# Kernel optimization log

Measured on AMD Instinct MI355X. Metric: run time of the kernel, lower is better.

The kernel has to match this reference:

```python
import jax, jax.numpy as jnp
import numpy as np

B, T, D = 4, 2048, 1024
H, K, V = 4, 256, 256        # head_k_dim = head_v_dim = hidden/num_heads
M, TOPK = 256, 4             # num_slots == head_k_dim
CHUNK = 64                   # scan checkpointing granularity
SCALE = K ** -0.5            # kernel default q scale


def setup_inputs() -> dict:
    key = jax.random.key(0)
    ks = jax.random.split(key, 10)
    s = lambda i, shape, sc: jax.random.normal(ks[i], shape, jnp.float32) * sc
    return {
        "hidden_states": s(0, (B, T, D), 1.0),
        "Wq": s(1, (D, H * K), D ** -0.5),
        "Wk": s(2, (D, H * K), D ** -0.5),
        "Wv": s(3, (D, H * V), D ** -0.5),
        "Wa": s(4, (D, H), D ** -0.5),
        "Wr": s(5, (D, H * M), D ** -0.5),
        "Wb": s(6, (D, H), D ** -0.5),
        "dt": jax.random.uniform(ks[7], (H,), jnp.float32, np.log(0.001), np.log(0.1)),
        "norm_w": jnp.ones((V,), jnp.float32),
        "Wo": s(8, (H * V, D), (H * V) ** -0.5),
    }


def _l2norm(x):
    return x * jax.lax.rsqrt(jnp.sum(x * x, axis=-1, keepdims=True) + 1e-6)


def _delta_scan(q, k, v, g, beta):
    """Gated delta-rule recurrence. Time-major inputs:
    q,k,g: [T,B,H,K]; v: [T,B,H,V]; beta: [T,B,H]. Returns o: [T,B,H,V]."""
    def step(S, inp):
        qt, kt, vt, gt, bt = inp
        S = S * jnp.exp(gt)[..., None]                              # diag decay on key dim
        err = vt - jnp.einsum('bhk,bhkv->bhv', kt, S)               # delta-rule error
        S = S + kt[..., None] * (bt[..., None] * err)[..., None, :]
        o = jnp.einsum('bhk,bhkv->bhv', qt, S)
        return S, o

    @jax.checkpoint
    def chunk_fn(S, inp):
        return jax.lax.scan(step, S, inp)

    nc = T // CHUNK
    inp = tuple(x.reshape((nc, CHUNK) + x.shape[1:]) for x in (q, k, v, g, beta))
    S0 = jnp.zeros((B, H, K, V), jnp.float32)
    _, o = jax.lax.scan(chunk_fn, S0, inp)                          # o: [nc,CHUNK,B,H,V]
    return o.reshape((T,) + o.shape[2:])


def reference(hidden_states, Wq, Wk, Wv, Wa, Wr, Wb, dt, norm_w, Wo):
    h = hidden_states
    q = jax.nn.silu(h @ Wq).reshape(B, T, H, K)
    k = jax.nn.silu(h @ Wk).reshape(B, T, H, K)
    v = jax.nn.silu(h @ Wv).reshape(B, T, H, V)
    a = -jax.nn.softplus(h @ Wa) * jnp.exp(dt)                      # [B,T,H] log-decay magnitude
    rt = (h @ Wr).reshape(B, T, H, M)
    beta = jax.nn.sigmoid(h @ Wb)                                   # [B,T,H]

    # noisy top-k slot routing (eval: no noise)
    m = jax.nn.sigmoid(rt)
    w, idx = jax.lax.top_k(m, TOPK)                                 # [B,T,H,TOPK]
    mask = jnp.sum(jax.nn.one_hot(idx, M, dtype=m.dtype) * w[..., None], axis=-2)
    r = mask / (jnp.sum(mask, axis=-1, keepdims=True) + 1e-6)
    g = a[..., None] * r                                            # [B,T,H,K] (M == K)

    k = k * (1.0 - jnp.exp(g))
    q = _l2norm(q) * SCALE
    k = _l2norm(k)

    tm = lambda x: jnp.moveaxis(x, 1, 0)
    o = _delta_scan(tm(q), tm(k), tm(v), tm(g), tm(beta))           # [T,B,H,V]
    o = jnp.moveaxis(o, 0, 1)                                       # [B,T,H,V]

    # RMSNorm on head_v_dim (fp32, eps 1e-5)
    o = o * jax.lax.rsqrt(jnp.mean(o * o, axis=-1, keepdims=True) + 1e-5) * norm_w
    return o.reshape(B, T, H * V) @ Wo
```

## Files before the change

### kernel.cpp

```cpp
#include <hip/hip_runtime.h>
#include <hip/hip_bf16.h>

#define TT 2048
#define BB 4
#define HH 4
#define DD 1024

using bf16x8 = __attribute__((ext_vector_type(8))) short;
using f32x4  = __attribute__((ext_vector_type(4))) float;

__device__ __forceinline__ float wave_sum(float x) {
#pragma unroll
  for (int off = 32; off >= 1; off >>= 1) x += __shfl_xor(x, off);
  return x;
}

__device__ __forceinline__ float siluf(float x) {
  return x / (1.f + expf(-x));
}

__device__ __forceinline__ unsigned short f2bf(float f) {
  unsigned u = __float_as_uint(f);
  u = (u + 0x7fffu + ((u >> 16) & 1u)) >> 16;
  return (unsigned short)u;
}
__device__ __forceinline__ float bf2f(unsigned short b) {
  return __uint_as_float(((unsigned)b) << 16);
}
__device__ __forceinline__ unsigned pack2(float a, float b) {
  return ((unsigned)f2bf(a)) | (((unsigned)f2bf(b)) << 16);
}

__device__ __forceinline__ void gload_lds16(const void* g, void* l) {
  __builtin_amdgcn_global_load_lds(
      (const __attribute__((address_space(1))) unsigned int*)g,
      (__attribute__((address_space(3))) unsigned int*)l, 16, 0, 0);
}

#define LBAR()                                              \
  do {                                                      \
    asm volatile("s_waitcnt lgkmcnt(0)" ::: "memory");      \
    __builtin_amdgcn_s_barrier();                           \
    __builtin_amdgcn_sched_barrier(0);                      \
  } while (0)

__global__ __launch_bounds__(256) void gemm_bt(const unsigned short* __restrict__ A,
                                               const unsigned short* __restrict__ Bt,
                                               float* __restrict__ C,
                                               int M, int N, int K) {
  __shared__ unsigned short As[128 * 64];
  __shared__ unsigned short Bs[128 * 64];
  const int tid = threadIdx.x;
  const int l = tid & 63;
  const int w = tid >> 6;
  const int wm = w >> 1, wn = w & 1;
  const int bid = blockIdx.x;
  const int nt = N >> 7;
  const int swz = (bid & 7) * ((int)gridDim.x >> 3) + (bid >> 3);
  const int m0 = (swz / nt) * 128, n0 = (swz % nt) * 128;

  f32x4 acc[4][4];
#pragma unroll
  for (int i = 0; i < 4; ++i)
#pragma unroll
    for (int j = 0; j < 4; ++j) acc[i][j] = (f32x4){0.f, 0.f, 0.f, 0.f};

  size_t asrc[4], bsrc[4];
  int ldst[4];
#pragma unroll
  for (int it = 0; it < 4; ++it) {
    int chunk = (it * 4 + w) * 64 + l;
    int row = chunk >> 3, s = chunk & 7;
    size_t soff = (size_t)row * K + ((s ^ (row & 7)) << 3);
    asrc[it] = (size_t)m0 * K + soff;
    bsrc[it] = (size_t)n0 * K + soff;
    ldst[it] = chunk * 8;
  }
  int ra_off[2][4], rb_off[2][4];
#pragma unroll
  for (int kh = 0; kh < 2; ++kh)
#pragma unroll
    for (int f = 0; f < 4; ++f) {
      int rowA = wm * 64 + f * 16 + (l & 15);
      ra_off[kh][f] = rowA * 128 + (((kh * 4 + (l >> 4)) ^ (rowA & 7)) << 4);
      int rowB = wn * 64 + f * 16 + (l & 15);
      rb_off[kh][f] = rowB * 128 + (((kh * 4 + (l >> 4)) ^ (rowB & 7)) << 4);
    }

  for (int k0 = 0; k0 < K; k0 += 64) {
    __syncthreads();
#pragma unroll
    for (int it = 0; it < 4; ++it) {
      gload_lds16(A + asrc[it] + k0, As + ldst[it] - l * 8);
      gload_lds16(Bt + bsrc[it] + k0, Bs + ldst[it] - l * 8);
    }
    __syncthreads();
#pragma unroll
    for (int kh = 0; kh < 2; ++kh) {
      bf16x8 af[4], bfv[4];
#pragma unroll
      for (int f = 0; f < 4; ++f) {
        af[f] = *(const bf16x8*)((const char*)As + ra_off[kh][f]);
        bfv[f] = *(const bf16x8*)((const char*)Bs + rb_off[kh][f]);
      }
#pragma unroll
      for (int i = 0; i < 4; ++i)
#pragma unroll
        for (int j = 0; j < 4; ++j)
          acc[i][j] = __builtin_amdgcn_mfma_f32_16x16x32_bf16(af[i], bfv[j],
                                                              acc[i][j], 0, 0, 0);
    }
  }
  const int cn = n0 + wn * 64 + (l & 15);
  const int rbase = m0 + wm * 64 + ((l >> 4) << 2);
#pragma unroll
  for (int i = 0; i < 4; ++i)
#pragma unroll
    for (int j = 0; j < 4; ++j)
#pragma unroll
      for (int r = 0; r < 4; ++r)
        C[(size_t)(rbase + i * 16 + r) * N + cn + j * 16] = acc[i][j][r];
}

__global__ __launch_bounds__(256) void gemm_bt3(const unsigned short* __restrict__ Ah,
                                                const unsigned short* __restrict__ Al,
                                                const unsigned short* __restrict__ Bh,
                                                const unsigned short* __restrict__ Bl,
                                                float* __restrict__ C,
                                                int M, int N, int K) {
  __shared__ unsigned short Ash[128 * 64];
  __shared__ unsigned short Asl[128 * 64];
  __shared__ unsigned short Bsh[128 * 64];
  __shared__ unsigned short Bsl[128 * 64];
  const int tid = threadIdx.x;
  const int l = tid & 63;
  const int w = tid >> 6;
  const int wm = w >> 1, wn = w & 1;
  const int bid = blockIdx.x;
  const int nt = N >> 7;
  const int swz = (bid & 7) * ((int)gridDim.x >> 3) + (bid >> 3);
  const int m0 = (swz / nt) * 128, n0 = (swz % nt) * 128;

  f32x4 acc[4][4];
#pragma unroll
  for (int i = 0; i < 4; ++i)
#pragma unroll
    for (int j = 0; j < 4; ++j) acc[i][j] = (f32x4){0.f, 0.f, 0.f, 0.f};

  size_t asrc[4], bsrc[4];
  int ldst[4];
#pragma unroll
  for (int it = 0; it < 4; ++it) {
    int chunk = (it * 4 + w) * 64 + l;
    int row = chunk >> 3, s = chunk & 7;
    size_t soff = (size_t)row * K + ((s ^ (row & 7)) << 3);
    asrc[it] = (size_t)m0 * K + soff;
    bsrc[it] = (size_t)n0 * K + soff;
    ldst[it] = chunk * 8;
  }
  int ra_off[2][4], rb_off[2][4];
#pragma unroll
  for (int kh = 0; kh < 2; ++kh)
#pragma unroll
    for (int f = 0; f < 4; ++f) {
      int rowA = wm * 64 + f * 16 + (l & 15);
      ra_off[kh][f] = rowA * 128 + (((kh * 4 + (l >> 4)) ^ (rowA & 7)) << 4);
      int rowB = wn * 64 + f * 16 + (l & 15);
      rb_off[kh][f] = rowB * 128 + (((kh * 4 + (l >> 4)) ^ (rowB & 7)) << 4);
    }

  for (int k0 = 0; k0 < K; k0 += 64) {
    __syncthreads();
#pragma unroll
    for (int it = 0; it < 4; ++it) {
      gload_lds16(Ah + asrc[it] + k0, Ash + ldst[it] - l * 8);
      gload_lds16(Al + asrc[it] + k0, Asl + ldst[it] - l * 8);
      gload_lds16(Bh + bsrc[it] + k0, Bsh + ldst[it] - l * 8);
      gload_lds16(Bl + bsrc[it] + k0, Bsl + ldst[it] - l * 8);
    }
    __syncthreads();
#pragma unroll
    for (int kh = 0; kh < 2; ++kh) {
      bf16x8 afh[4], bfh[4], tmp[4];
#pragma unroll
      for (int f = 0; f < 4; ++f) {
        afh[f] = *(const bf16x8*)((const char*)Ash + ra_off[kh][f]);
        bfh[f] = *(const bf16x8*)((const char*)Bsh + rb_off[kh][f]);
      }
#pragma unroll
      for (int i = 0; i < 4; ++i)
#pragma unroll
        for (int j = 0; j < 4; ++j)
          acc[i][j] = __builtin_amdgcn_mfma_f32_16x16x32_bf16(afh[i], bfh[j],
                                                              acc[i][j], 0, 0, 0);
#pragma unroll
      for (int f = 0; f < 4; ++f)
        tmp[f] = *(const bf16x8*)((const char*)Asl + ra_off[kh][f]);
#pragma unroll
      for (int i = 0; i < 4; ++i)
#pragma unroll
        for (int j = 0; j < 4; ++j)
          acc[i][j] = __builtin_amdgcn_mfma_f32_16x16x32_bf16(tmp[i], bfh[j],
                                                              acc[i][j], 0, 0, 0);
#pragma unroll
      for (int f = 0; f < 4; ++f)
        tmp[f] = *(const bf16x8*)((const char*)Bsl + rb_off[kh][f]);
#pragma unroll
      for (int i = 0; i < 4; ++i)
#pragma unroll
        for (int j = 0; j < 4; ++j)
          acc[i][j] = __builtin_amdgcn_mfma_f32_16x16x32_bf16(afh[i], tmp[j],
                                                              acc[i][j], 0, 0, 0);
    }
  }
  const int cn = n0 + wn * 64 + (l & 15);
  const int rbase = m0 + wm * 64 + ((l >> 4) << 2);
#pragma unroll
  for (int i = 0; i < 4; ++i)
#pragma unroll
    for (int j = 0; j < 4; ++j)
#pragma unroll
      for (int r = 0; r < 4; ++r)
        C[(size_t)(rbase + i * 16 + r) * N + cn + j * 16] = acc[i][j][r];
}

__global__ __launch_bounds__(256) void cast2_bf16_kernel(const float* __restrict__ in,
                                                         unsigned short* __restrict__ hi,
                                                         unsigned short* __restrict__ lo) {
  const size_t i = ((size_t)blockIdx.x * 256 + threadIdx.x) * 4;
  float4 x = *(const float4*)(in + i);
  ushort4 h4, l4;
  h4.x = f2bf(x.x); l4.x = f2bf(x.x - bf2f(h4.x));
  h4.y = f2bf(x.y); l4.y = f2bf(x.y - bf2f(h4.y));
  h4.z = f2bf(x.z); l4.z = f2bf(x.z - bf2f(h4.z));
  h4.w = f2bf(x.w); l4.w = f2bf(x.w - bf2f(h4.w));
  *(ushort4*)(hi + i) = h4;
  *(ushort4*)(lo + i) = l4;
}

__global__ __launch_bounds__(256) void tcast_kernel(const float* __restrict__ W,
                                                    unsigned short* __restrict__ WT,
                                                    int R, int C) {
  __shared__ float tile[32][33];
  const int tx = threadIdx.x, ty = threadIdx.y;
  const int c0 = blockIdx.x * 32, r0 = blockIdx.y * 32;
#pragma unroll
  for (int i = 0; i < 4; ++i)
    tile[ty + 8 * i][tx] = W[(size_t)(r0 + ty + 8 * i) * C + c0 + tx];
  __syncthreads();
#pragma unroll
  for (int i = 0; i < 4; ++i)
    WT[(size_t)(c0 + ty + 8 * i) * R + r0 + tx] = f2bf(tile[tx][ty + 8 * i]);
}

__global__ __launch_bounds__(256) void tcast2_kernel(const float* __restrict__ W,
                                                     unsigned short* __restrict__ WTh,
                                                     unsigned short* __restrict__ WTl,
                                                     int R, int C) {
  __shared__ float tile[32][33];
  const int tx = threadIdx.x, ty = threadIdx.y;
  const int c0 = blockIdx.x * 32, r0 = blockIdx.y * 32;
#pragma unroll
  for (int i = 0; i < 4; ++i)
    tile[ty + 8 * i][tx] = W[(size_t)(r0 + ty + 8 * i) * C + c0 + tx];
  __syncthreads();
#pragma unroll
  for (int i = 0; i < 4; ++i) {
    float x = tile[tx][ty + 8 * i];
    unsigned short h = f2bf(x);
    WTh[(size_t)(c0 + ty + 8 * i) * R + r0 + tx] = h;
    WTl[(size_t)(c0 + ty + 8 * i) * R + r0 + tx] = f2bf(x - bf2f(h));
  }
}

__global__ __launch_bounds__(256) void routing_kernel(
    const float* __restrict__ hidden, const float* __restrict__ Wa,
    const float* __restrict__ Wb, const float* __restrict__ dt,
    const float* __restrict__ rproj, float* __restrict__ qkv,
    float* __restrict__ gbuf, float* __restrict__ betaT) {
  const int row = blockIdx.x;
  const int b = row >> 11;
  const int t = row & (TT - 1);
  const int h = threadIdx.x >> 6;
  const int l = threadIdx.x & 63;
  const size_t base_q = (size_t)row * 3072 + h * 256;
  const size_t base_k = base_q + 1024;
  const size_t base_v = base_q + 2048;
  const size_t base_r = (size_t)row * DD + h * 256;

  const float* hrow = hidden + (size_t)row * DD;
  float aa = 0.f, bb = 0.f;
#pragma unroll
  for (int i = 0; i < 16; ++i) {
    float hv = hrow[l + 64 * i];
    aa = fmaf(hv, Wa[(l + 64 * i) * HH + h], aa);
    bb = fmaf(hv, Wb[(l + 64 * i) * HH + h], bb);
  }
  aa = wave_sum(aa);
  bb = wave_sum(bb);
  float sp = (aa > 20.f) ? aa : log1pf(expf(aa));
  float a_ = -sp * expf(dt[h]);
  float beta = 1.f / (1.f + expf(-bb));
  const int bh = b * HH + h;
  if (l == 0) betaT[(size_t)bh * TT + t] = beta;

  float4 rt4 = *(const float4*)(rproj + base_r + l * 4);
  float rv[4] = {rt4.x, rt4.y, rt4.z, rt4.w};
  int used = 0;
  int widx[4];
  float wsig[4], wg[4], wkfac[4];
#pragma unroll
  for (int it = 0; it < 4; ++it) {
    float bv = -3.4e38f;
    int bi = 0x7fffffff;
#pragma unroll
    for (int c = 0; c < 4; ++c) {
      bool ok = !(used & (1 << c));
      float v = rv[c];
      if (ok && (v > bv)) {
        bv = v;
        bi = l * 4 + c;
      }
    }
#pragma unroll
    for (int off = 32; off >= 1; off >>= 1) {
      float ov = __shfl_xor(bv, off);
      int oi = __shfl_xor(bi, off);
      if (ov > bv || (ov == bv && oi < bi)) {
        bv = ov;
        bi = oi;
      }
    }
    widx[it] = bi;
    wsig[it] = 1.f / (1.f + expf(-bv));
    if ((bi >> 2) == l) used |= 1 << (bi & 3);
  }
  float wsum = wsig[0] + wsig[1] + wsig[2] + wsig[3] + 1e-6f;
#pragma unroll
  for (int it = 0; it < 4; ++it) {
    float g = a_ * (wsig[it] / wsum);
    wg[it] = g;
    wkfac[it] = 1.f - expf(g);
  }

  float4 kv4 = *(const float4*)(qkv + base_k + l * 4);
  float kvv[4] = {kv4.x, kv4.y, kv4.z, kv4.w};
  float kmask[4], ddv[4];
#pragma unroll
  for (int c = 0; c < 4; ++c) {
    int slot = l * 4 + c;
    float f = 0.f, d = 0.f;
#pragma unroll
    for (int it = 0; it < 4; ++it) {
      bool hit = (slot == widx[it]);
      f = hit ? wkfac[it] : f;
      d = hit ? wg[it] : d;
    }
    kmask[c] = siluf(kvv[c]) * f;
    ddv[c] = d;
  }
  float ss = kmask[0] * kmask[0] + kmask[1] * kmask[1] + kmask[2] * kmask[2] +
             kmask[3] * kmask[3];
  ss = wave_sum(ss);
  float kn = rsqrtf(ss + 1e-6f);
  *(float4*)(qkv + base_k + l * 4) =
      make_float4(kmask[0] * kn, kmask[1] * kn, kmask[2] * kn, kmask[3] * kn);
  *(float4*)(gbuf + ((size_t)bh * TT + t) * 256 + l * 4) =
      make_float4(ddv[0], ddv[1], ddv[2], ddv[3]);

  float4 qv4 = *(const float4*)(qkv + base_q + l * 4);
  float qs[4] = {siluf(qv4.x), siluf(qv4.y), siluf(qv4.z), siluf(qv4.w)};
  float qss = qs[0] * qs[0] + qs[1] * qs[1] + qs[2] * qs[2] + qs[3] * qs[3];
  qss = wave_sum(qss);
  float qn = rsqrtf(qss + 1e-6f) * 0.0625f;
  *(float4*)(qkv + base_q + l * 4) =
      make_float4(qs[0] * qn, qs[1] * qn, qs[2] * qn, qs[3] * qn);

  float4 vv4 = *(const float4*)(qkv + base_v + l * 4);
  *(float4*)(qkv + base_v + l * 4) =
      make_float4(siluf(vv4.x), siluf(vv4.y), siluf(vv4.z), siluf(vv4.w));
}

__global__ __launch_bounds__(256) void phaseA_kernel(
    const float* __restrict__ qkv,
    float* __restrict__ expcG,
    const float* __restrict__ betaT, unsigned short* __restrict__ TinvB,
    unsigned short* __restrict__ AB, unsigned short* __restrict__ Wg,
    unsigned short* __restrict__ Qg, unsigned short* __restrict__ XTg) {
  __shared__ unsigned short XB[64 * 256];
  __shared__ unsigned short QW[128 * 256];
  __shared__ float Mb[64 * 68];
  const int bid = blockIdx.x;
  const int bh = bid >> 5, c = bid & 31;
  const int b = bh >> 2, h = bh & 3;
  const int t0 = c * 64;
  const int tid = threadIdx.x;
  const int w = tid >> 6, l = tid & 63;
  const int ln = l & 15, lg = l >> 4;

  {
    float cacc = 0.f;
    const int slot = tid >> 3, byt = tid & 7;
#pragma unroll 4
    for (int i = 0; i < 64; ++i) {
      size_t ga = ((size_t)bh * TT + t0 + i) * 256 + tid;
      size_t pq = (size_t)(b * TT + t0 + i) * 3072 + h * 256 + tid;
      cacc += expcG[ga];
      float e = expf(cacc);
      float ei = __builtin_amdgcn_rcpf(e);
      float qv = qkv[pq];
      float kv = qkv[pq + 1024];
      unsigned short wb = f2bf(kv * e);
      unsigned short qb = f2bf(qv * e);
      unsigned short xb = f2bf(kv * ei);
      Wg[ga] = wb;
      Qg[ga] = qb;
      int sw = ((slot ^ (i & 7)) << 3) + byt;
      XB[i * 256 + sw] = xb;
      QW[i * 256 + sw] = qb;
      QW[(i + 64) * 256 + sw] = wb;
      if (i == 63) expcG[ga] = e;
    }
  }
  __syncthreads();

  f32x4 acc[2][4];
#pragma unroll
  for (int tr = 0; tr < 2; ++tr)
#pragma unroll
    for (int tc = 0; tc < 4; ++tc) acc[tr][tc] = (f32x4){0.f, 0.f, 0.f, 0.f};
  const int R0 = w * 32;
#pragma unroll
  for (int kt = 0; kt < 8; ++kt) {
    const int ks = kt * 4 + lg;
    const int ra0 = R0 + ln, ra1 = R0 + 16 + ln;
    bf16x8 a0 = *(const bf16x8*)&QW[ra0 * 256 + ((ks ^ (ra0 & 7)) << 3)];
    bf16x8 a1 = *(const bf16x8*)&QW[ra1 * 256 + ((ks ^ (ra1 & 7)) << 3)];
#pragma unroll
    for (int tc = 0; tc < 4; ++tc) {
      const int br = tc * 16 + ln;
      bf16x8 bf_ = *(const bf16x8*)&XB[br * 256 + ((ks ^ (br & 7)) << 3)];
      acc[0][tc] = __builtin_amdgcn_mfma_f32_16x16x32_bf16(a0, bf_, acc[0][tc], 0, 0, 0);
      acc[1][tc] = __builtin_amdgcn_mfma_f32_16x16x32_bf16(a1, bf_, acc[1][tc], 0, 0, 0);
    }
  }
  const size_t gb = (((size_t)bh * 32 + c) << 12);
  if (w < 2) {
#pragma unroll
    for (int tr = 0; tr < 2; ++tr)
#pragma unroll
      for (int tc = 0; tc < 4; ++tc)
#pragma unroll
        for (int r = 0; r < 4; ++r) {
          int i = R0 + tr * 16 + lg * 4 + r;
          int s = tc * 16 + ln;
          AB[gb + i * 64 + s] = (s <= i) ? f2bf(acc[tr][tc][r]) : (unsigned short)0;
        }
  } else {
#pragma unroll
    for (int tr = 0; tr < 2; ++tr)
#pragma unroll
      for (int tc = 0; tc < 4; ++tc)
#pragma unroll
        for (int r = 0; r < 4; ++r) {
          int i = R0 - 64 + tr * 16 + lg * 4 + r;
          Mb[i * 68 + tc * 16 + ln] = acc[tr][tc][r];
        }
  }
  __syncthreads();

  if (w == 0) {
    float tcol[64];
#pragma unroll
    for (int i = 0; i < 64; ++i) {
      float bi = betaT[(size_t)bh * TT + t0 + i];
      float a_ = (l == i) ? 1.f : 0.f;
#pragma unroll
      for (int s = 0; s < i; ++s)
        a_ = fmaf(-bi * Mb[i * 68 + s], tcol[s], a_);
      tcol[i] = a_;
    }
#pragma unroll
    for (int s = 0; s < 64; ++s) Mb[s * 68 + l] = tcol[s];
  } else {
    const int kk1 = tid - 64;
#pragma unroll 1
    for (int pass = 0; pass < 2; ++pass) {
      if (pass == 1 && kk1 >= 64) break;
      const int k = (pass == 0) ? kk1 : (192 + kk1);
      unsigned short* dst = XTg + ((size_t)bh * 256 + k) * TT + t0;
      const int kslot = k >> 3, kb = k & 7;
#pragma unroll 1
      for (int jq = 0; jq < 8; ++jq) {
        unsigned short e[8];
#pragma unroll
        for (int j = 0; j < 8; ++j) {
          int t = jq * 8 + j;
          e[j] = XB[t * 256 + (((kslot ^ (t & 7)) << 3) + kb)];
        }
        uint4 o;
        o.x = ((unsigned)e[0]) | (((unsigned)e[1]) << 16);
        o.y = ((unsigned)e[2]) | (((unsigned)e[3]) << 16);
        o.z = ((unsigned)e[4]) | (((unsigned)e[5]) << 16);
        o.w = ((unsigned)e[6]) | (((unsigned)e[7]) << 16);
        *(uint4*)(dst + jq * 8) = o;
      }
    }
  }
  __syncthreads();
  {
    const int i = tid >> 2;
    const int sb = (tid & 3) * 16;
#pragma unroll
    for (int mq = 0; mq < 4; ++mq) {
      float v0 = Mb[i * 68 + sb + mq * 4 + 0];
      float v1 = Mb[i * 68 + sb + mq * 4 + 1];
      float v2 = Mb[i * 68 + sb + mq * 4 + 2];
      float v3 = Mb[i * 68 + sb + mq * 4 + 3];
      uint2 p;
      p.x = pack2(v0, v1);
      p.y = pack2(v2, v3);
      *(uint2*)(TinvB + gb + (size_t)i * 64 + sb + mq * 4) = p;
    }
  }
}

__global__ __launch_bounds__(256) void chunk_scan_kernel(
    const unsigned short* __restrict__ Wg, const unsigned short* __restrict__ Qg,
    const unsigned short* __restrict__ XTg, const unsigned short* __restrict__ Tb,
    const unsigned short* __restrict__ Ab, const float* __restrict__ qkv,
    const float* __restrict__ expcG, const float* __restrict__ betaT,
    float* __restrict__ obuf) {
  __shared__ unsigned short ShL[16 * 256];
  __shared__ unsigned short SlL[16 * 256];
  __shared__ unsigned short R2bL[16 * 64];
  __shared__ unsigned short UbL[16 * 64];
  const int bid = blockIdx.x;
  const int bh = bid & 15, slice = bid >> 4;
  const int b = bh >> 2, h = bh & 3;
  const int tid = threadIdx.x;
  const int w = tid >> 6;
  const int l = tid & 63;
  const int ln = l & 15, lg = l >> 4;

  const unsigned short* Wbh = Wg + (size_t)bh * TT * 256;
  const unsigned short* Qbh = Qg + (size_t)bh * TT * 256;
  const unsigned short* XTbh = XTg + (size_t)bh * 256 * TT;
  const unsigned short* Tbh = Tb + (size_t)bh * 32 * 4096;
  const unsigned short* Abh = Ab + (size_t)bh * 32 * 4096;
  const float* betabh = betaT + (size_t)bh * TT;
  const float* ebh = expcG + (size_t)bh * TT * 256;

  f32x4 S0 = {0.f, 0.f, 0.f, 0.f}, S1 = S0, S2 = S0, S3 = S0;

  const int ru_off =
      ln * 64 + ((((w * 2) + (lg >> 1)) ^ (ln & 7)) << 3) + (lg & 1) * 4;

  bf16x8 wA[8], qA[8], wB[8], qB[8];
  float4 vA, bA, vB, bB;

#define LOADWQV(W_, Q_, V_, B_, c_)                                            \
  {                                                                            \
    const int t0_ = (c_) * 64;                                                 \
    _Pragma("unroll") for (int kt = 0; kt < 8; ++kt) {                         \
      const size_t arow =                                                      \
          (size_t)(t0_ + w * 16 + ln) * 256 + kt * 32 + lg * 8;                \
      W_[kt] = *(const bf16x8*)(Wbh + arow);                                   \
      Q_[kt] = *(const bf16x8*)(Qbh + arow);                                   \
    }                                                                          \
    const size_t vrow = (size_t)(b * TT + t0_ + w * 16 + lg * 4) * 3072 +      \
                        2048 + h * 256 + slice * 16 + ln;                      \
    V_.x = qkv[vrow];                                                          \
    V_.y = qkv[vrow + 3072];                                                   \
    V_.z = qkv[vrow + 2 * 3072];                                               \
    V_.w = qkv[vrow + 3 * 3072];                                               \
    B_ = *(const float4*)(betabh + t0_ + w * 16 + lg * 4);                     \
  }

#define SSTORE(S_, E_, mt_)                                                    \
  {                                                                            \
    S_[0] *= E_.x;                                                             \
    S_[1] *= E_.y;                                                             \
    S_[2] *= E_.z;                                                             \
    S_[3] *= E_.w;                                                             \
    ushort4 hp, lp;                                                            \
    hp.x = f2bf(S_[0]); lp.x = f2bf(S_[0] - bf2f(hp.x));                       \
    hp.y = f2bf(S_[1]); lp.y = f2bf(S_[1] - bf2f(hp.y));                       \
    hp.z = f2bf(S_[2]); lp.z = f2bf(S_[2] - bf2f(hp.z));                       \
    hp.w = f2bf(S_[3]); lp.w = f2bf(S_[3] - bf2f(hp.w));                       \
    const int so_ = ln * 256 +                                                 \
                    ((((w * 8) + (mt_)*2 + (lg >> 1)) ^ ln) << 3) +            \
                    (lg & 1) * 4;                                              \
    *(ushort4*)(&ShL[so_]) = hp;                                               \
    *(ushort4*)(&SlL[so_]) = lp;                                               \
  }

#define CHUNK(Wc, Qc, Vc, Bc, Wn, Qn, Vn, Bn, c_)                              \
  {                                                                            \
    const int c = (c_);                                                        \
    const size_t tb_base = (size_t)c * 4096 + (w * 16 + ln) * 64 + lg * 8;     \
    bf16x8 tf0 = *(const bf16x8*)(Tbh + tb_base);                              \
    bf16x8 tf1 = *(const bf16x8*)(Tbh + tb_base + 32);                         \
    bf16x8 af0 = *(const bf16x8*)(Abh + tb_base);                              \
    bf16x8 af1 = *(const bf16x8*)(Abh + tb_base + 32);                         \
    const size_t xb = (size_t)(w * 64 + ln) * TT + c * 64 + lg * 8;            \
    bf16x8 xf0a = *(const bf16x8*)(XTbh + xb);                                 \
    bf16x8 xf0b = *(const bf16x8*)(XTbh + xb + 32);                            \
    bf16x8 xf1a = *(const bf16x8*)(XTbh + xb + 16 * TT);                       \
    bf16x8 xf1b = *(const bf16x8*)(XTbh + xb + 16 * TT + 32);                  \
    bf16x8 xf2a = *(const bf16x8*)(XTbh + xb + 32 * TT);                       \
    bf16x8 xf2b = *(const bf16x8*)(XTbh + xb + 32 * TT + 32);                  \
    bf16x8 xf3a = *(const bf16x8*)(XTbh + xb + 48 * TT);                       \
    bf16x8 xf3b = *(const bf16x8*)(XTbh + xb + 48 * TT + 32);                  \
    const float* ebase = ebh + (size_t)(c * 64 + 63) * 256 + w * 64 + lg * 4;  \
    float4 eL0 = *(const float4*)(ebase);                                      \
    float4 eL1 = *(const float4*)(ebase + 16);                                 \
    float4 eL2 = *(const float4*)(ebase + 32);                                 \
    float4 eL3 = *(const float4*)(ebase + 48);                                 \
    f32x4 rhs = {0.f, 0.f, 0.f, 0.f}, oq = {0.f, 0.f, 0.f, 0.f};               \
    if (c > 0) {                                                               \
      _Pragma("unroll") for (int kt = 0; kt < 8; ++kt) {                       \
        const int sro = ln * 256 + (((kt * 4 + lg) ^ ln) << 3);                \
        bf16x8 sh = *(const bf16x8*)(&ShL[sro]);                               \
        bf16x8 sl = *(const bf16x8*)(&SlL[sro]);                               \
        rhs = __builtin_amdgcn_mfma_f32_16x16x32_bf16(Wc[kt], sh, rhs, 0, 0, 0); \
        rhs = __builtin_amdgcn_mfma_f32_16x16x32_bf16(Wc[kt], sl, rhs, 0, 0, 0); \
        oq = __builtin_amdgcn_mfma_f32_16x16x32_bf16(Qc[kt], sh, oq, 0, 0, 0); \
        oq = __builtin_amdgcn_mfma_f32_16x16x32_bf16(Qc[kt], sl, oq, 0, 0, 0); \
      }                                                                        \
    }                                                                          \
    if (c + 1 < 32) LOADWQV(Wn, Qn, Vn, Bn, c + 1);                            \
    {                                                                          \
      ushort4 r2p;                                                             \
      r2p.x = f2bf(Bc.x * (Vc.x - rhs[0]));                                    \
      r2p.y = f2bf(Bc.y * (Vc.y - rhs[1]));                                    \
      r2p.z = f2bf(Bc.z * (Vc.z - rhs[2]));                                    \
      r2p.w = f2bf(Bc.w * (Vc.w - rhs[3]));                                    \
      *(ushort4*)(&R2bL[ru_off]) = r2p;                                        \
    }                                                                          \
    LBAR();                                                                    \
    {                                                                          \
      bf16x8 rf0 = *(const bf16x8*)(&R2bL[ln * 64 + (((0 + lg) ^ (ln & 7)) << 3)]); \
      bf16x8 rf1 = *(const bf16x8*)(&R2bL[ln * 64 + (((4 + lg) ^ (ln & 7)) << 3)]); \
      f32x4 u = {0.f, 0.f, 0.f, 0.f};                                          \
      u = __builtin_amdgcn_mfma_f32_16x16x32_bf16(tf0, rf0, u, 0, 0, 0);       \
      u = __builtin_amdgcn_mfma_f32_16x16x32_bf16(tf1, rf1, u, 0, 0, 0);       \
      ushort4 up;                                                              \
      up.x = f2bf(u[0]);                                                       \
      up.y = f2bf(u[1]);                                                       \
      up.z = f2bf(u[2]);                                                       \
      up.w = f2bf(u[3]);                                                       \
      *(ushort4*)(&UbL[ru_off]) = up;                                          \
    }                                                                          \
    LBAR();                                                                    \
    bf16x8 uf0 = *(const bf16x8*)(&UbL[ln * 64 + (((0 + lg) ^ (ln & 7)) << 3)]); \
    bf16x8 uf1 = *(const bf16x8*)(&UbL[ln * 64 + (((4 + lg) ^ (ln & 7)) << 3)]); \
    {                                                                          \
      f32x4 o = oq;                                                            \
      o = __builtin_amdgcn_mfma_f32_16x16x32_bf16(af0, uf0, o, 0, 0, 0);       \
      o = __builtin_amdgcn_mfma_f32_16x16x32_bf16(af1, uf1, o, 0, 0, 0);       \
      const size_t orow =                                                      \
          ((size_t)(b * TT + c * 64 + w * 16 + lg * 4) * HH + h) * 256 +       \
          slice * 16 + ln;                                                     \
      obuf[orow] = o[0];                                                       \
      obuf[orow + HH * 256] = o[1];                                            \
      obuf[orow + 2 * HH * 256] = o[2];                                        \
      obuf[orow + 3 * HH * 256] = o[3];                                        \
    }                                                                          \
    S0 = __builtin_amdgcn_mfma_f32_16x16x32_bf16(xf0a, uf0, S0, 0, 0, 0);      \
    S0 = __builtin_amdgcn_mfma_f32_16x16x32_bf16(xf0b, uf1, S0, 0, 0, 0);      \
    S1 = __builtin_amdgcn_mfma_f32_16x16x32_bf16(xf1a, uf0, S1, 0, 0, 0);      \
    S1 = __builtin_amdgcn_mfma_f32_16x16x32_bf16(xf1b, uf1, S1, 0, 0, 0);      \
    S2 = __builtin_amdgcn_mfma_f32_16x16x32_bf16(xf2a, uf0, S2, 0, 0, 0);      \
    S2 = __builtin_amdgcn_mfma_f32_16x16x32_bf16(xf2b, uf1, S2, 0, 0, 0);      \
    S3 = __builtin_amdgcn_mfma_f32_16x16x32_bf16(xf3a, uf0, S3, 0, 0, 0);      \
    S3 = __builtin_amdgcn_mfma_f32_16x16x32_bf16(xf3b, uf1, S3, 0, 0, 0);      \
    SSTORE(S0, eL0, 0);                                                        \
    SSTORE(S1, eL1, 1);                                                        \
    SSTORE(S2, eL2, 2);                                                        \
    SSTORE(S3, eL3, 3);                                                        \
    LBAR();                                                                    \
  }

  LOADWQV(wA, qA, vA, bA, 0);
  for (int cc = 0; cc < 32; cc += 2) {
    CHUNK(wA, qA, vA, bA, wB, qB, vB, bB, cc);
    CHUNK(wB, qB, vB, bB, wA, qA, vA, bA, cc + 1);
  }
#undef CHUNK
#undef SSTORE
#undef LOADWQV
}

__global__ __launch_bounds__(256) void rmsnorm_bf16_kernel(
    const float* __restrict__ o, const float* __restrict__ w,
    unsigned short* __restrict__ out) {
  const int row = blockIdx.x;
  const int l = threadIdx.x & 63;
  const size_t base = (size_t)row * DD + (threadIdx.x >> 6) * 256 + l * 4;
  float4 x = *(const float4*)(o + base);
  float ss = x.x * x.x + x.y * x.y + x.z * x.z + x.w * x.w;
  ss = wave_sum(ss);
  float sc = rsqrtf(ss * (1.f / 256.f) + 1e-5f);
  float4 wv = *(const float4*)(w + l * 4);
  ushort4 o4;
  o4.x = f2bf(x.x * sc * wv.x);
  o4.y = f2bf(x.y * sc * wv.y);
  o4.z = f2bf(x.z * sc * wv.z);
  o4.w = f2bf(x.w * sc * wv.w);
  *(ushort4*)(out + base) = o4;
}

extern "C" void kernel_launch(void* const* d_in, const int* in_sizes, int n_in,
                              void* d_out, int out_size, void* d_ws,
                              size_t ws_size, hipStream_t stream) {
  const float* hidden = (const float*)d_in[0];
  const float* Wq = (const float*)d_in[1];
  const float* Wk = (const float*)d_in[2];
  const float* Wv = (const float*)d_in[3];
  const float* Wa = (const float*)d_in[4];
  const float* Wr = (const float*)d_in[5];
  const float* Wb = (const float*)d_in[6];
  const float* dt = (const float*)d_in[7];
  const float* norm_w = (const float*)d_in[8];
  const float* Wo = (const float*)d_in[9];
  float* out = (float*)d_out;

  const size_t NP = (size_t)BB * TT * DD;
  float* ws = (float*)d_ws;
  float* qkv = ws;
  float* gbuf = ws + 3 * NP;
  unsigned short* hbf = (unsigned short*)(ws + 4 * NP);
  unsigned short* wT = (unsigned short*)(ws + 4 * NP + NP / 2);
  unsigned short* WT0 = wT;
  unsigned short* WT1 = wT + 1048576;
  unsigned short* WT2 = wT + 2 * 1048576;
  unsigned short* WT3 = wT + 3 * 1048576;
  unsigned short* WT4 = wT + 4 * 1048576;
  unsigned short* WT5 = wT + 5 * 1048576;
  float* betaT = ws + 4 * NP + NP / 2 + 3 * 1024 * 1024;
  float* after_beta = betaT + 16 * TT;
  unsigned short* Qg = (unsigned short*)after_beta;
  unsigned short* XTg = Qg + NP;
  unsigned short* Ab = XTg + NP;
  unsigned short* Wgb = hbf;
  unsigned short* Tbb = WT4;
  unsigned short* hlo = (unsigned short*)qkv;
  float* rproj = out;

  dim3 bt(256);
  cast2_bf16_kernel<<<8192, 256, 0, stream>>>(hidden, hbf, hlo);
  dim3 tg(32, 32), tb(32, 8);
  tcast2_kernel<<<tg, tb, 0, stream>>>(Wr, WT4, WT5, 1024, 1024);
  tcast_kernel<<<tg, tb, 0, stream>>>(Wq, WT0, 1024, 1024);
  tcast_kernel<<<tg, tb, 0, stream>>>(Wk, WT1, 1024, 1024);
  tcast_kernel<<<tg, tb, 0, stream>>>(Wv, WT2, 1024, 1024);
  tcast_kernel<<<tg, tb, 0, stream>>>(Wo, WT3, 1024, 1024);

  gemm_bt3<<<512, bt, 0, stream>>>(hbf, hlo, WT4, WT5, rproj, 8192, 1024, 1024);
  gemm_bt<<<1536, bt, 0, stream>>>(hbf, WT0, qkv, 8192, 3072, 1024);

  routing_kernel<<<8192, 256, 0, stream>>>(hidden, Wa, Wb, dt, rproj, qkv,
                                           gbuf, betaT);
  phaseA_kernel<<<512, 256, 0, stream>>>(qkv, gbuf, betaT, Tbb, Ab, Wgb, Qg,
                                         XTg);
  chunk_scan_kernel<<<256, 256, 0, stream>>>(Wgb, Qg, XTg, Tbb, Ab, qkv, gbuf,
                                             betaT, out);
  rmsnorm_bf16_kernel<<<8192, 256, 0, stream>>>(out, norm_w, hbf);
  gemm_bt<<<512, bt, 0, stream>>>(hbf, WT3, out, 8192, 1024, 1024);
}
```

Baseline: 444.6 us.

## Make chunk scan wave-local to drop intra-chunk barriers, double-buffer W and state in LDS

In the chunk scan, every wave now computes the full 64-row delta-rule residual and U transform for its own slice into private LDS buffers. This replaces the two block-wide barriers per chunk with wave-local lgkmcnt fences. The W tile is staged asynchronously into double-buffered LDS with global_load_lds, and the bf16 hi/lo state is double-buffered, so only one __syncthreads per chunk remains. The cost is four times redundant W·S MFMA work and LDS traffic per wave, plus more LDS footprint, which may lower occupancy.

```diff
diff --git a/kernel.cpp b/kernel.cpp
--- a/kernel.cpp
+++ b/kernel.cpp
@@ -37,10 +37,9 @@
       (__attribute__((address_space(3))) unsigned int*)l, 16, 0, 0);
 }
 
-#define LBAR()                                              \
+#define WFENCE()                                            \
   do {                                                      \
     asm volatile("s_waitcnt lgkmcnt(0)" ::: "memory");      \
-    __builtin_amdgcn_s_barrier();                           \
     __builtin_amdgcn_sched_barrier(0);                      \
   } while (0)
 
@@ -531,10 +530,11 @@
     const unsigned short* __restrict__ Ab, const float* __restrict__ qkv,
     const float* __restrict__ expcG, const float* __restrict__ betaT,
     float* __restrict__ obuf) {
-  __shared__ unsigned short ShL[16 * 256];
-  __shared__ unsigned short SlL[16 * 256];
-  __shared__ unsigned short R2bL[16 * 64];
-  __shared__ unsigned short UbL[16 * 64];
+  __shared__ unsigned short WL[2][64 * 256];
+  __shared__ unsigned short ShL[2][16 * 256];
+  __shared__ unsigned short SlL[2][16 * 256];
+  __shared__ unsigned short R2L[4][16 * 64];
+  __shared__ unsigned short UL[4][16 * 64];
   const int bid = blockIdx.x;
   const int bh = bid & 15, slice = bid >> 4;
   const int b = bh >> 2, h = bh & 3;
@@ -553,143 +553,171 @@
 
   f32x4 S0 = {0.f, 0.f, 0.f, 0.f}, S1 = S0, S2 = S0, S3 = S0;
 
-  const int ru_off =
-      ln * 64 + ((((w * 2) + (lg >> 1)) ^ (ln & 7)) << 3) + (lg & 1) * 4;
-
-  bf16x8 wA[8], qA[8], wB[8], qB[8];
-  float4 vA, bA, vB, bB;
-
-#define LOADWQV(W_, Q_, V_, B_, c_)                                            \
+  int wsrc_off[8], wdst[8];
+#pragma unroll
+  for (int i = 0; i < 8; ++i) {
+    int chunk = i * 256 + tid;
+    int row = chunk >> 5, sd = chunk & 31;
+    wsrc_off[i] = row * 256 + ((sd ^ (row & 7)) << 3);
+    wdst[i] = chunk * 8 - l * 8;
+  }
+
+#define STAGEW(buf, cc)                                                        \
   {                                                                            \
-    const int t0_ = (c_) * 64;                                                 \
-    _Pragma("unroll") for (int kt = 0; kt < 8; ++kt) {                         \
-      const size_t arow =                                                      \
-          (size_t)(t0_ + w * 16 + ln) * 256 + kt * 32 + lg * 8;                \
-      W_[kt] = *(const bf16x8*)(Wbh + arow);                                   \
-      Q_[kt] = *(const bf16x8*)(Qbh + arow);                                   \
-    }                                                                          \
-    const size_t vrow = (size_t)(b * TT + t0_ + w * 16 + lg * 4) * 3072 +      \
-                        2048 + h * 256 + slice * 16 + ln;                      \
-    V_.x = qkv[vrow];                                                          \
-    V_.y = qkv[vrow + 3072];                                                   \
-    V_.z = qkv[vrow + 2 * 3072];                                               \
-    V_.w = qkv[vrow + 3 * 3072];                                               \
-    B_ = *(const float4*)(betabh + t0_ + w * 16 + lg * 4);                     \
-  }
-
+    const unsigned short* wsrc_ = Wbh + (size_t)(cc) * 64 * 256;               \
+    _Pragma("unroll") for (int i_ = 0; i_ < 8; ++i_)                           \
+        gload_lds16(wsrc_ + wsrc_off[i_], (unsigned short*)WL[buf] + wdst[i_]); \
+  }
+
+  STAGEW(0, 0);
+  __syncthreads();
+
+  for (int c = 0; c < 32; ++c) {
+    const int cur = c & 1;
+    if (c + 1 < 32) STAGEW(cur ^ 1, c + 1);
+    const size_t tA = (size_t)c * 4096;
+    bf16x8 tf[4][2];
+#pragma unroll
+    for (int ut = 0; ut < 4; ++ut)
+#pragma unroll
+      for (int kt = 0; kt < 2; ++kt)
+        tf[ut][kt] = *(const bf16x8*)(Tbh + tA + (ut * 16 + ln) * 64 +
+                                      kt * 32 + lg * 8);
+    bf16x8 af0 = *(const bf16x8*)(Abh + tA + (w * 16 + ln) * 64 + lg * 8);
+    bf16x8 af1 = *(const bf16x8*)(Abh + tA + (w * 16 + ln) * 64 + 32 + lg * 8);
+    float4 Vv[4], Bt4[4];
+#pragma unroll
+    for (int mt = 0; mt < 4; ++mt) {
+      const size_t vrow = (size_t)(b * TT + c * 64 + mt * 16 + lg * 4) * 3072 +
+                          2048 + h * 256 + slice * 16 + ln;
+      Vv[mt].x = qkv[vrow];
+      Vv[mt].y = qkv[vrow + 3072];
+      Vv[mt].z = qkv[vrow + 2 * 3072];
+      Vv[mt].w = qkv[vrow + 3 * 3072];
+      Bt4[mt] = *(const float4*)(betabh + c * 64 + mt * 16 + lg * 4);
+    }
+    f32x4 rhs[4];
+#pragma unroll
+    for (int mt = 0; mt < 4; ++mt) rhs[mt] = (f32x4){0.f, 0.f, 0.f, 0.f};
+    if (c > 0) {
+#pragma unroll
+      for (int kt = 0; kt < 8; ++kt) {
+        const int sro = ln * 256 + (((kt * 4 + lg) ^ ln) << 3);
+        bf16x8 sh = *(const bf16x8*)(&ShL[cur][sro]);
+        bf16x8 sl = *(const bf16x8*)(&SlL[cur][sro]);
+#pragma unroll
+        for (int mt = 0; mt < 4; ++mt) {
+          bf16x8 wf = *(const bf16x8*)(
+              &WL[cur][(mt * 16 + ln) * 256 + (((kt * 4 + lg) ^ (ln & 7)) << 3)]);
+          rhs[mt] = __builtin_amdgcn_mfma_f32_16x16x32_bf16(wf, sh, rhs[mt], 0, 0, 0);
+          rhs[mt] = __builtin_amdgcn_mfma_f32_16x16x32_bf16(wf, sl, rhs[mt], 0, 0, 0);
+        }
+      }
+    }
+#pragma unroll
+    for (int mt = 0; mt < 4; ++mt) {
+      ushort4 p;
+      p.x = f2bf(Bt4[mt].x * (Vv[mt].x - rhs[mt][0]));
+      p.y = f2bf(Bt4[mt].y * (Vv[mt].y - rhs[mt][1]));
+      p.z = f2bf(Bt4[mt].z * (Vv[mt].z - rhs[mt][2]));
+      p.w = f2bf(Bt4[mt].w * (Vv[mt].w - rhs[mt][3]));
+      const int off =
+          ln * 64 + ((((mt * 2) + (lg >> 1)) ^ (ln & 7)) << 3) + (lg & 1) * 4;
+      *(ushort4*)(&R2L[w][off]) = p;
+    }
+    bf16x8 xf[4][2];
+#pragma unroll
+    for (int st = 0; st < 4; ++st)
+#pragma unroll
+      for (int kt = 0; kt < 2; ++kt)
+        xf[st][kt] = *(const bf16x8*)(XTbh + (size_t)(w * 64 + st * 16 + ln) * TT +
+                                      c * 64 + kt * 32 + lg * 8);
+    float4 eL[4];
+#pragma unroll
+    for (int st = 0; st < 4; ++st)
+      eL[st] = *(const float4*)(ebh + (size_t)(c * 64 + 63) * 256 + w * 64 +
+                                st * 16 + lg * 4);
+    bf16x8 qf[8];
+#pragma unroll
+    for (int kt = 0; kt < 8; ++kt)
+      qf[kt] = *(const bf16x8*)(Qbh + (size_t)(c * 64 + w * 16 + ln) * 256 +
+                                kt * 32 + lg * 8);
+    WFENCE();
+    {
+      bf16x8 rf0 = *(const bf16x8*)(&R2L[w][ln * 64 + (((0 + lg) ^ (ln & 7)) << 3)]);
+      bf16x8 rf1 = *(const bf16x8*)(&R2L[w][ln * 64 + (((4 + lg) ^ (ln & 7)) << 3)]);
+#pragma unroll
+      for (int ut = 0; ut < 4; ++ut) {
+        f32x4 u = {0.f, 0.f, 0.f, 0.f};
+        u = __builtin_amdgcn_mfma_f32_16x16x32_bf16(tf[ut][0], rf0, u, 0, 0, 0);
+        u = __builtin_amdgcn_mfma_f32_16x16x32_bf16(tf[ut][1], rf1, u, 0, 0, 0);
+        ushort4 p;
+        p.x = f2bf(u[0]); p.y = f2bf(u[1]); p.z = f2bf(u[2]); p.w = f2bf(u[3]);
+        const int off =
+            ln * 64 + ((((ut * 2) + (lg >> 1)) ^ (ln & 7)) << 3) + (lg & 1) * 4;
+        *(ushort4*)(&UL[w][off]) = p;
+      }
+    }
+    WFENCE();
+    bf16x8 uf0 = *(const bf16x8*)(&UL[w][ln * 64 + (((0 + lg) ^ (ln & 7)) << 3)]);
+    bf16x8 uf1 = *(const bf16x8*)(&UL[w][ln * 64 + (((4 + lg) ^ (ln & 7)) << 3)]);
+    f32x4 oq = {0.f, 0.f, 0.f, 0.f};
+    if (c > 0) {
+#pragma unroll
+      for (int kt = 0; kt < 8; ++kt) {
+        const int sro = ln * 256 + (((kt * 4 + lg) ^ ln) << 3);
+        bf16x8 sh = *(const bf16x8*)(&ShL[cur][sro]);
+        bf16x8 sl = *(const bf16x8*)(&SlL[cur][sro]);
+        oq = __builtin_amdgcn_mfma_f32_16x16x32_bf16(qf[kt], sh, oq, 0, 0, 0);
+        oq = __builtin_amdgcn_mfma_f32_16x16x32_bf16(qf[kt], sl, oq, 0, 0, 0);
+      }
+    }
+    {
+      f32x4 o = oq;
+      o = __builtin_amdgcn_mfma_f32_16x16x32_bf16(af0, uf0, o, 0, 0, 0);
+      o = __builtin_amdgcn_mfma_f32_16x16x32_bf16(af1, uf1, o, 0, 0, 0);
+      const size_t orow =
+          ((size_t)(b * TT + c * 64 + w * 16 + lg * 4) * HH + h) * 256 +
+          slice * 16 + ln;
+      obuf[orow] = o[0];
+      obuf[orow + HH * 256] = o[1];
+      obuf[orow + 2 * HH * 256] = o[2];
+      obuf[orow + 3 * HH * 256] = o[3];
+    }
+    S0 = __builtin_amdgcn_mfma_f32_16x16x32_bf16(xf[0][0], uf0, S0, 0, 0, 0);
+    S0 = __builtin_amdgcn_mfma_f32_16x16x32_bf16(xf[0][1], uf1, S0, 0, 0, 0);
+    S1 = __builtin_amdgcn_mfma_f32_16x16x32_bf16(xf[1][0], uf0, S1, 0, 0, 0);
+    S1 = __builtin_amdgcn_mfma_f32_16x16x32_bf16(xf[1][1], uf1, S1, 0, 0, 0);
+    S2 = __builtin_amdgcn_mfma_f32_16x16x32_bf16(xf[2][0], uf0, S2, 0, 0, 0);
+    S2 = __builtin_amdgcn_mfma_f32_16x16x32_bf16(xf[2][1], uf1, S2, 0, 0, 0);
+    S3 = __builtin_amdgcn_mfma_f32_16x16x32_bf16(xf[3][0], uf0, S3, 0, 0, 0);
+    S3 = __builtin_amdgcn_mfma_f32_16x16x32_bf16(xf[3][1], uf1, S3, 0, 0, 0);
+    const int nxt = cur ^ 1;
 #define SSTORE(S_, E_, mt_)                                                    \
-  {                                                                            \
-    S_[0] *= E_.x;                                                             \
-    S_[1] *= E_.y;                                                             \
-    S_[2] *= E_.z;                                                             \
-    S_[3] *= E_.w;                                                             \
-    ushort4 hp, lp;                                                            \
-    hp.x = f2bf(S_[0]); lp.x = f2bf(S_[0] - bf2f(hp.x));                       \
-    hp.y = f2bf(S_[1]); lp.y = f2bf(S_[1] - bf2f(hp.y));                       \
-    hp.z = f2bf(S_[2]); lp.z = f2bf(S_[2] - bf2f(hp.z));                       \
-    hp.w = f2bf(S_[3]); lp.w = f2bf(S_[3] - bf2f(hp.w));                       \
-    const int so_ = ln * 256 +                                                 \
-                    ((((w * 8) + (mt_)*2 + (lg >> 1)) ^ ln) << 3) +            \
-                    (lg & 1) * 4;                                              \
-    *(ushort4*)(&ShL[so_]) = hp;                                               \
-    *(ushort4*)(&SlL[so_]) = lp;                                               \
-  }
-
-#define CHUNK(Wc, Qc, Vc, Bc, Wn, Qn, Vn, Bn, c_)                              \
-  {                                                                            \
-    const int c = (c_);                                                        \
-    const size_t tb_base = (size_t)c * 4096 + (w * 16 + ln) * 64 + lg * 8;     \
-    bf16x8 tf0 = *(const bf16x8*)(Tbh + tb_base);                              \
-    bf16x8 tf1 = *(const bf16x8*)(Tbh + tb_base + 32);                         \
-    bf16x8 af0 = *(const bf16x8*)(Abh + tb_base);                              \
-    bf16x8 af1 = *(const bf16x8*)(Abh + tb_base + 32);                         \
-    const size_t xb = (size_t)(w * 64 + ln) * TT + c * 64 + lg * 8;            \
-    bf16x8 xf0a = *(const bf16x8*)(XTbh + xb);                                 \
-    bf16x8 xf0b = *(const bf16x8*)(XTbh + xb + 32);                            \
-    bf16x8 xf1a = *(const bf16x8*)(XTbh + xb + 16 * TT);                       \
-    bf16x8 xf1b = *(const bf16x8*)(XTbh + xb + 16 * TT + 32);                  \
-    bf16x8 xf2a = *(const bf16x8*)(XTbh + xb + 32 * TT);                       \
-    bf16x8 xf2b = *(const bf16x8*)(XTbh + xb + 32 * TT + 32);                  \
-    bf16x8 xf3a = *(const bf16x8*)(XTbh + xb + 48 * TT);                       \
-    bf16x8 xf3b = *(const bf16x8*)(XTbh + xb + 48 * TT + 32);                  \
-    const float* ebase = ebh + (size_t)(c * 64 + 63) * 256 + w * 64 + lg * 4;  \
-    float4 eL0 = *(const float4*)(ebase);                                      \
-    float4 eL1 = *(const float4*)(ebase + 16);                                 \
-    float4 eL2 = *(const float4*)(ebase + 32);                                 \
-    float4 eL3 = *(const float4*)(ebase + 48);                                 \
-    f32x4 rhs = {0.f, 0.f, 0.f, 0.f}, oq = {0.f, 0.f, 0.f, 0.f};               \
-    if (c > 0) {                                                               \
-      _Pragma("unroll") for (int kt = 0; kt < 8; ++kt) {                       \
-        const int sro = ln * 256 + (((kt * 4 + lg) ^ ln) << 3);                \
-        bf16x8 sh = *(const bf16x8*)(&ShL[sro]);                               \
-        bf16x8 sl = *(const bf16x8*)(&SlL[sro]);                               \
-        rhs = __builtin_amdgcn_mfma_f32_16x16x32_bf16(Wc[kt], sh, rhs, 0, 0, 0); \
-        rhs = __builtin_amdgcn_mfma_f32_16x16x32_bf16(Wc[kt], sl, rhs, 0, 0, 0); \
-        oq = __builtin_amdgcn_mfma_f32_16x16x32_bf16(Qc[kt], sh, oq, 0, 0, 0); \
-        oq = __builtin_amdgcn_mfma_f32_16x16x32_bf16(Qc[kt], sl, oq, 0, 0, 0); \
-      }                                                                        \
-    }                                                                          \
-    if (c + 1 < 32) LOADWQV(Wn, Qn, Vn, Bn, c + 1);                            \
     {                                                                          \
-      ushort4 r2p;                                                             \
-      r2p.x = f2bf(Bc.x * (Vc.x - rhs[0]));                                    \
-      r2p.y = f2bf(Bc.y * (Vc.y - rhs[1]));                                    \
-      r2p.z = f2bf(Bc.z * (Vc.z - rhs[2]));                                    \
-      r2p.w = f2bf(Bc.w * (Vc.w - rhs[3]));                                    \
-      *(ushort4*)(&R2bL[ru_off]) = r2p;                                        \
-    }                                                                          \
-    LBAR();                                                                    \
-    {                                                                          \
-      bf16x8 rf0 = *(const bf16x8*)(&R2bL[ln * 64 + (((0 + lg) ^ (ln & 7)) << 3)]); \
-      bf16x8 rf1 = *(const bf16x8*)(&R2bL[ln * 64 + (((4 + lg) ^ (ln & 7)) << 3)]); \
-      f32x4 u = {0.f, 0.f, 0.f, 0.f};                                          \
-      u = __builtin_amdgcn_mfma_f32_16x16x32_bf16(tf0, rf0, u, 0, 0, 0);       \
-      u = __builtin_amdgcn_mfma_f32_16x16x32_bf16(tf1, rf1, u, 0, 0, 0);       \
-      ushort4 up;                                                              \
-      up.x = f2bf(u[0]);                                                       \
-      up.y = f2bf(u[1]);                                                       \
-      up.z = f2bf(u[2]);                                                       \
-      up.w = f2bf(u[3]);                                                       \
-      *(ushort4*)(&UbL[ru_off]) = up;                                          \
-    }                                                                          \
-    LBAR();                                                                    \
-    bf16x8 uf0 = *(const bf16x8*)(&UbL[ln * 64 + (((0 + lg) ^ (ln & 7)) << 3)]); \
-    bf16x8 uf1 = *(const bf16x8*)(&UbL[ln * 64 + (((4 + lg) ^ (ln & 7)) << 3)]); \
-    {                                                                          \
-      f32x4 o = oq;                                                            \
-      o = __builtin_amdgcn_mfma_f32_16x16x32_bf16(af0, uf0, o, 0, 0, 0);       \
-      o = __builtin_amdgcn_mfma_f32_16x16x32_bf16(af1, uf1, o, 0, 0, 0);       \
-      const size_t orow =                                                      \
-          ((size_t)(b * TT + c * 64 + w * 16 + lg * 4) * HH + h) * 256 +       \
-          slice * 16 + ln;                                                     \
-      obuf[orow] = o[0];                                                       \
-      obuf[orow + HH * 256] = o[1];                                            \
-      obuf[orow + 2 * HH * 256] = o[2];                                        \
-      obuf[orow + 3 * HH * 256] = o[3];                                        \
-    }                                                                          \
-    S0 = __builtin_amdgcn_mfma_f32_16x16x32_bf16(xf0a, uf0, S0, 0, 0, 0);      \
-    S0 = __builtin_amdgcn_mfma_f32_16x16x32_bf16(xf0b, uf1, S0, 0, 0, 0);      \
-    S1 = __builtin_amdgcn_mfma_f32_16x16x32_bf16(xf1a, uf0, S1, 0, 0, 0);      \
-    S1 = __builtin_amdgcn_mfma_f32_16x16x32_bf16(xf1b, uf1, S1, 0, 0, 0);      \
-    S2 = __builtin_amdgcn_mfma_f32_16x16x32_bf16(xf2a, uf0, S2, 0, 0, 0);      \
-    S2 = __builtin_amdgcn_mfma_f32_16x16x32_bf16(xf2b, uf1, S2, 0, 0, 0);      \
-    S3 = __builtin_amdgcn_mfma_f32_16x16x32_bf16(xf3a, uf0, S3, 0, 0, 0);      \
-    S3 = __builtin_amdgcn_mfma_f32_16x16x32_bf16(xf3b, uf1, S3, 0, 0, 0);      \
-    SSTORE(S0, eL0, 0);                                                        \
-    SSTORE(S1, eL1, 1);                                                        \
-    SSTORE(S2, eL2, 2);                                                        \
-    SSTORE(S3, eL3, 3);                                                        \
-    LBAR();                                                                    \
-  }
-
-  LOADWQV(wA, qA, vA, bA, 0);
-  for (int cc = 0; cc < 32; cc += 2) {
-    CHUNK(wA, qA, vA, bA, wB, qB, vB, bB, cc);
-    CHUNK(wB, qB, vB, bB, wA, qA, vA, bA, cc + 1);
-  }
-#undef CHUNK
+      S_[0] *= E_.x;                                                           \
+      S_[1] *= E_.y;                                                           \
+      S_[2] *= E_.z;                                                           \
+      S_[3] *= E_.w;                                                           \
+      ushort4 hp, lp;                                                          \
+      hp.x = f2bf(S_[0]); lp.x = f2bf(S_[0] - bf2f(hp.x));                     \
+      hp.y = f2bf(S_[1]); lp.y = f2bf(S_[1] - bf2f(hp.y));                     \
+      hp.z = f2bf(S_[2]); lp.z = f2bf(S_[2] - bf2f(hp.z));                     \
+      hp.w = f2bf(S_[3]); lp.w = f2bf(S_[3] - bf2f(hp.w));                     \
+      const int so_ = ln * 256 +                                               \
+                      ((((w * 8) + (mt_)*2 + (lg >> 1)) ^ ln) << 3) +          \
+                      (lg & 1) * 4;                                            \
+      *(ushort4*)(&ShL[nxt][so_]) = hp;                                        \
+      *(ushort4*)(&SlL[nxt][so_]) = lp;                                        \
+    }
+    SSTORE(S0, eL[0], 0);
+    SSTORE(S1, eL[1], 1);
+    SSTORE(S2, eL[2], 2);
+    SSTORE(S3, eL[3], 3);
 #undef SSTORE
-#undef LOADWQV
+    __syncthreads();
+  }
+#undef STAGEW
 }
 
 __global__ __launch_bounds__(256) void rmsnorm_bf16_kernel(
```

Measured after the change: 502.5 us. +13.0%, slower.
